# Kernel optimization log

Hardware: AMD Instinct MI355X
Metric: run time of the kernel (lower is better)

The kernel has to match this reference:

```python
import jax, jax.numpy as jnp
import numpy as np

B, T, C, H, N, FF = 2, 1024, 2048, 32, 64, 8192
DIV = 8.0  # head_size_divisor
LAYER_ID, N_LAYER = 1, 24
EPS = 1e-5


def _layer_norm(x, g, b):
    m = x.mean(-1, keepdims=True)
    v = x.var(-1, keepdims=True)
    return (x - m) / jnp.sqrt(v + EPS) * g + b


def _group_norm(x, g, b):
    # GroupNorm(H, C) applied per token: normalize each head's N channels
    xg = x.reshape(B, T, H, N)
    m = xg.mean(-1, keepdims=True)
    v = xg.var(-1, keepdims=True)
    xn = ((xg - m) / jnp.sqrt(v + EPS)).reshape(B, T, C)
    return xn * g + b


def _time_shift(x):
    # xx[t] = x[t-1], xx[0] = 0
    return jnp.pad(x, ((0, 0), (1, 0), (0, 0)))[:, :-1]


def _wkv5(r, k, v, w, u):
    # r,k,v: [B,T,H,N]; w,u: [H,N]. Linear recurrence with per-channel decay.
    decay = jnp.exp(-jnp.exp(w))            # [H,N]
    dec = decay[None, :, :, None]           # broadcast over B and v-dim
    uu = u[None, :, :, None]
    rs = jnp.moveaxis(r, 1, 0)              # [T,B,H,N]
    ks = jnp.moveaxis(k, 1, 0)
    vs = jnp.moveaxis(v, 1, 0)

    def step(state, inp):                   # state: [B,H,N,N] (k-dim i, v-dim j)
        rt, kt, vt = inp
        kv = kt[..., :, None] * vt[..., None, :]          # [B,H,N,N]
        y = jnp.einsum('bhi,bhij->bhj', rt, uu * kv + state)
        return dec * state + kv, y

    state0 = jnp.zeros((B, H, N, N), r.dtype)
    _, ys = jax.lax.scan(step, state0, (rs, ks, vs))
    return jnp.moveaxis(ys, 0, 1).reshape(B, T, C)


def _forward(x, ln1_g, ln1_b, ln2_g, ln2_b,
             tm_k, tm_v, tm_r, tm_g, time_decay, time_faaaa,
             Wr, Wk, Wv, Wg, Wo, lnx_g, lnx_b,
             fm_k, fm_r, Wkey, Wrec, Wval):
    # ---- TimeMix ----
    xl = _layer_norm(x, ln1_g, ln1_b)
    xx = _time_shift(xl)
    xk = xl * tm_k + xx * (1 - tm_k)
    xv = xl * tm_v + xx * (1 - tm_v)
    xr = xl * tm_r + xx * (1 - tm_r)
    xg = xl * tm_g + xx * (1 - tm_g)
    r = (xr @ Wr).reshape(B, T, H, N)
    k = (xk @ Wk).reshape(B, T, H, N)
    v = (xv @ Wv).reshape(B, T, H, N)
    g = jax.nn.silu(xg @ Wg)
    att = _wkv5(r, k, v, time_decay, time_faaaa)
    att = _group_norm(att / DIV, lnx_g, lnx_b)
    x = x + (att * g) @ Wo
    # ---- ChannelMix ----
    xl2 = _layer_norm(x, ln2_g, ln2_b)
    xx2 = _time_shift(xl2)
    ck = xl2 * fm_k + xx2 * (1 - fm_k)
    cr = xl2 * fm_r + xx2 * (1 - fm_r)
    kk = jnp.square(jax.nn.relu(ck @ Wkey))
    kv = kk @ Wval
    return x + jax.nn.sigmoid(cr @ Wrec) * kv


def setup_inputs() -> dict:
    key = jax.random.key(0)
    ks = jax.random.split(key, 9)
    r01 = LAYER_ID / (N_LAYER - 1)
    r1a0 = 1.0 - LAYER_ID / N_LAYER
    ddd = (np.arange(C, dtype=np.float64) / C)[None, None, :]
    dec = np.array([-6 + 5 * (n / (C - 1)) ** (0.7 + 1.3 * r01) for n in range(C)])
    faa = np.array([r01 * (1 - n / (C - 1)) + ((n + 1) % 3 - 1) * 0.1 for n in range(C)])
    f32 = lambda a: jnp.asarray(a, jnp.float32)
    w = lambda k_, i, o: jax.random.normal(k_, (i, o), jnp.float32) * (i ** -0.5)
    return {
        'x': jax.random.normal(ks[0], (B, T, C), jnp.float32),
        'ln1_g': jnp.ones((C,), jnp.float32), 'ln1_b': jnp.zeros((C,), jnp.float32),
        'ln2_g': jnp.ones((C,), jnp.float32), 'ln2_b': jnp.zeros((C,), jnp.float32),
        'tm_k': f32(ddd ** r1a0), 'tm_v': f32(ddd ** r1a0 + 0.3 * r01),
        'tm_r': f32(ddd ** (0.5 * r1a0)), 'tm_g': f32(ddd ** (0.5 * r1a0)),
        'time_decay': f32(dec.reshape(H, N)), 'time_faaaa': f32(faa.reshape(H, N)),
        'Wr': w(ks[1], C, C), 'Wk': w(ks[2], C, C), 'Wv': w(ks[3], C, C),
        'Wg': w(ks[4], C, C), 'Wo': w(ks[5], C, C),
        'lnx_g': jnp.ones((C,), jnp.float32), 'lnx_b': jnp.zeros((C,), jnp.float32),
        'fm_k': f32(ddd ** r1a0), 'fm_r': f32(ddd ** r1a0),
        'Wkey': w(ks[6], C, FF), 'Wrec': w(ks[7], C, C), 'Wval': w(ks[8], FF, C),
    }


def reference(x, ln1_g, ln1_b, ln2_g, ln2_b,
              tm_k, tm_v, tm_r, tm_g, time_decay, time_faaaa,
              Wr, Wk, Wv, Wg, Wo, lnx_g, lnx_b,
              fm_k, fm_r, Wkey, Wrec, Wval):
    return _forward(x, ln1_g, ln1_b, ln2_g, ln2_b,
                    tm_k, tm_v, tm_r, tm_g, time_decay, time_faaaa,
                    Wr, Wk, Wv, Wg, Wo, lnx_g, lnx_b,
                    fm_k, fm_r, Wkey, Wrec, Wval)
```

## Files before the change

### kernel.cpp

```cpp
#include <hip/hip_runtime.h>
#include <stdint.h>

#define BB 2
#define TT 1024
#define CC 2048
#define HH 32
#define NNH 64
#define FFD 8192
#define MTOT (BB*TT)
#define LNEPS 1e-5f
#define LOG2E 1.44269504088896340736f

typedef __attribute__((ext_vector_type(8))) __bf16 bf16x8;
typedef __attribute__((ext_vector_type(4))) float f32x4;

#define USE_GLL 1
typedef __attribute__((address_space(1))) void GAS;
typedef __attribute__((address_space(3))) void LAS;

__device__ inline void gload_lds16(const uint16_t* g, uint16_t* l) {
#if USE_GLL
  __builtin_amdgcn_global_load_lds((GAS*)g, (LAS*)l, 16, 0, 0);
#else
  *(uint4*)l = *(const uint4*)g;
#endif
}

__device__ inline float bf2f(uint32_t u) {
  union { uint32_t i; float f; } v; v.i = u << 16; return v.f;
}
__device__ inline uint16_t f2bf(float f) {
  union { float f; uint32_t i; } v; v.f = f;
  uint32_t r = v.i + 0x7FFFu + ((v.i >> 16) & 1u);
  return (uint16_t)(r >> 16);
}
__device__ inline void unpack8(uint4 d, float* v) {
  v[0] = bf2f(d.x & 0xffffu); v[1] = bf2f(d.x >> 16);
  v[2] = bf2f(d.y & 0xffffu); v[3] = bf2f(d.y >> 16);
  v[4] = bf2f(d.z & 0xffffu); v[5] = bf2f(d.z >> 16);
  v[6] = bf2f(d.w & 0xffffu); v[7] = bf2f(d.w >> 16);
}
__device__ inline uint4 pack8(const float* v) {
  uint4 d;
  d.x = (uint32_t)f2bf(v[0]) | ((uint32_t)f2bf(v[1]) << 16);
  d.y = (uint32_t)f2bf(v[2]) | ((uint32_t)f2bf(v[3]) << 16);
  d.z = (uint32_t)f2bf(v[4]) | ((uint32_t)f2bf(v[5]) << 16);
  d.w = (uint32_t)f2bf(v[6]) | ((uint32_t)f2bf(v[7]) << 16);
  return d;
}

__device__ inline void load8f(const void* p, size_t idx, int fl, float* v) {
  if (fl) {
    const float* q = (const float*)p + idx;
    float4 a = *(const float4*)q; float4 b = *(const float4*)(q + 4);
    v[0]=a.x; v[1]=a.y; v[2]=a.z; v[3]=a.w; v[4]=b.x; v[5]=b.y; v[6]=b.z; v[7]=b.w;
  } else {
    unpack8(*(const uint4*)((const uint16_t*)p + idx), v);
  }
}
__device__ inline float load1f(const void* p, size_t idx, int fl) {
  return fl ? ((const float*)p)[idx] : bf2f(((const uint16_t*)p)[idx]);
}

__global__ void probe_kernel(const uint16_t* __restrict__ x, int* __restrict__ flag) {
  int tid = threadIdx.x;
  float m = 0.f;
  for (int i = tid; i < 4096; i += 64) {
    float a = fabsf(bf2f(x[i]));
    if (a > m) m = a;
  }
  for (int o = 32; o; o >>= 1) { float t = __shfl_down(m, o); if (t > m) m = t; }
  if (tid == 0) *flag = (m > 1e6f) ? 1 : 0;
}

template<int INMODE>
__global__ __launch_bounds__(256) void ln_kernel(const void* __restrict__ x,
    const void* __restrict__ g, const void* __restrict__ b,
    uint16_t* __restrict__ out, const int* __restrict__ dflag)
{
  int fl = *dflag;
  int row = blockIdx.x;
  int tid = threadIdx.x;
  int lane = tid & 63, wave = tid >> 6;
  size_t base = (size_t)row * CC + (size_t)tid * 8;
  float v[8];
  if constexpr (INMODE == 1) {
    const float* q = (const float*)x + base;
    float4 a = *(const float4*)q; float4 c = *(const float4*)(q + 4);
    v[0]=a.x; v[1]=a.y; v[2]=a.z; v[3]=a.w; v[4]=c.x; v[5]=c.y; v[6]=c.z; v[7]=c.w;
  } else {
    load8f(x, base, fl, v);
  }
  float s = 0.f, s2 = 0.f;
  #pragma unroll
  for (int j = 0; j < 8; j++) { s += v[j]; s2 += v[j] * v[j]; }
  for (int o = 32; o; o >>= 1) { s += __shfl_down(s, o); s2 += __shfl_down(s2, o); }
  __shared__ float red[8];
  if (lane == 0) { red[wave] = s; red[wave + 4] = s2; }
  __syncthreads();
  s  = red[0] + red[1] + red[2] + red[3];
  s2 = red[4] + red[5] + red[6] + red[7];
  float mean = s * (1.0f / CC);
  float var  = s2 * (1.0f / CC) - mean * mean;
  float rstd = rsqrtf(fmaxf(var, 0.f) + LNEPS);
  float gj[8], bj[8];
  load8f(g, (size_t)tid * 8, fl, gj);
  load8f(b, (size_t)tid * 8, fl, bj);
  float o8[8];
  #pragma unroll
  for (int j = 0; j < 8; j++) o8[j] = (v[j] - mean) * rstd * gj[j] + bj[j];
  *(uint4*)(out + base) = pack8(o8);
}

__global__ __launch_bounds__(256) void mix4_kernel(const uint16_t* __restrict__ xl,
    const void* __restrict__ tmr, const void* __restrict__ tmk,
    const void* __restrict__ tmv, const void* __restrict__ tmg,
    uint16_t* __restrict__ out, const int* __restrict__ dflag)
{
  int fl = *dflag;
  uint32_t idx = ((uint32_t)blockIdx.x * 256u + threadIdx.x) * 8u;
  uint32_t c = idx & (CC - 1);
  uint32_t row = idx >> 11;
  uint32_t t = row & (TT - 1);
  float xv[8], pv[8];
  unpack8(*(const uint4*)(xl + idx), xv);
  if (t) { unpack8(*(const uint4*)(xl + idx - CC), pv); }
  else   { for (int j = 0; j < 8; j++) pv[j] = 0.f; }
  const void* tms[4] = { tmr, tmk, tmv, tmg };
  const size_t SL = (size_t)MTOT * CC;
  #pragma unroll
  for (int a = 0; a < 4; a++) {
    float tm[8], o[8];
    load8f(tms[a], c, fl, tm);
    #pragma unroll
    for (int j = 0; j < 8; j++) o[j] = xv[j] * tm[j] + pv[j] * (1.f - tm[j]);
    *(uint4*)(out + a * SL + idx) = pack8(o);
  }
}

__global__ __launch_bounds__(256) void mix2_kernel(const uint16_t* __restrict__ xl,
    const void* __restrict__ tk, const void* __restrict__ tr,
    uint16_t* __restrict__ ok, uint16_t* __restrict__ orr,
    const int* __restrict__ dflag)
{
  int fl = *dflag;
  uint32_t idx = ((uint32_t)blockIdx.x * 256u + threadIdx.x) * 8u;
  uint32_t c = idx & (CC - 1);
  uint32_t row = idx >> 11;
  uint32_t t = row & (TT - 1);
  float xv[8], pv[8], tm[8], o[8];
  unpack8(*(const uint4*)(xl + idx), xv);
  if (t) { unpack8(*(const uint4*)(xl + idx - CC), pv); }
  else   { for (int j = 0; j < 8; j++) pv[j] = 0.f; }
  load8f(tk, c, fl, tm);
  #pragma unroll
  for (int j = 0; j < 8; j++) o[j] = xv[j] * tm[j] + pv[j] * (1.f - tm[j]);
  *(uint4*)(ok + idx) = pack8(o);
  load8f(tr, c, fl, tm);
  #pragma unroll
  for (int j = 0; j < 8; j++) o[j] = xv[j] * tm[j] + pv[j] * (1.f - tm[j]);
  *(uint4*)(orr + idx) = pack8(o);
}

__device__ inline void transpose_tile(const void* W, uint16_t* WT, int Kd, int Nd,
                                      int n0, int k0, int fl, int tid)
{
  __shared__ __align__(16) uint16_t tile[64][66];
  int r = tid >> 3, s = tid & 7;
  #pragma unroll
  for (int p = 0; p < 2; p++) {
    int row = p * 32 + r;
    float tv[8];
    load8f(W, (size_t)(k0 + row) * Nd + n0 + s * 8, fl, tv);
    uint16_t* t = &tile[row][s * 8];
    #pragma unroll
    for (int e = 0; e < 8; e++) t[e] = f2bf(tv[e]);
  }
  __syncthreads();
  #pragma unroll
  for (int p = 0; p < 2; p++) {
    int row = p * 32 + r;
    uint16_t tmp[8];
    #pragma unroll
    for (int e = 0; e < 8; e++) tmp[e] = tile[s * 8 + e][row];
    uint4 o;
    o.x = (uint32_t)tmp[0] | ((uint32_t)tmp[1] << 16);
    o.y = (uint32_t)tmp[2] | ((uint32_t)tmp[3] << 16);
    o.z = (uint32_t)tmp[4] | ((uint32_t)tmp[5] << 16);
    o.w = (uint32_t)tmp[6] | ((uint32_t)tmp[7] << 16);
    *(uint4*)(WT + (size_t)(n0 + row) * Kd + k0 + s * 8) = o;
  }
}

__global__ __launch_bounds__(256) void transpose_kernel(const void* __restrict__ W,
    uint16_t* __restrict__ WT, int Kd, int Nd, const int* __restrict__ dflag)
{
  transpose_tile(W, WT, Kd, Nd, blockIdx.x * 64, blockIdx.y * 64, *dflag, threadIdx.x);
}

__global__ __launch_bounds__(256) void transpose4_kernel(
    const void* __restrict__ W0, const void* __restrict__ W1,
    const void* __restrict__ W2, const void* __restrict__ W3,
    uint16_t* __restrict__ WT, const int* __restrict__ dflag)
{
  const void* Ws[4] = { W0, W1, W2, W3 };
  int z = blockIdx.z;
  transpose_tile(Ws[z], WT + (size_t)z * CC * CC, CC, CC,
                 blockIdx.x * 64, blockIdx.y * 64, *dflag, threadIdx.x);
}

enum { EPI_RESID = 2, EPI_RKVG = 6, EPI_FF2 = 7, EPI_PART = 8 };

template<int EPI>
__global__ __launch_bounds__(256, 2) void gemm_kernel(
    const uint16_t* __restrict__ Ain, const uint16_t* __restrict__ BTin,
    void* __restrict__ Cout, int N, int Kstride, int Kloop,
    const void* __restrict__ auxA, const float* __restrict__ auxf,
    const uint16_t* __restrict__ A2in, const uint16_t* __restrict__ BT2in,
    void* __restrict__ C2out, const int* __restrict__ dflag)
{
  const uint16_t* A  = Ain;
  const uint16_t* BT = BTin;
  uint16_t* co16 = (uint16_t*)Cout;
  float*    co32 = (float*)Cout;
  int fl = 0;
  if constexpr (EPI == EPI_RESID) fl = *dflag;
  bool silu = false, sigm = false;
  int bx = blockIdx.x;
  int N_ = N;
  int n0 = bx * 128;
  if constexpr (EPI == EPI_RKVG) {
    int z = blockIdx.z;
    A    += (size_t)z * MTOT * CC;
    BT   += (size_t)z * CC * CC;
    co16 += (size_t)z * MTOT * CC;
    silu = (z == 3);
  }
  if constexpr (EPI == EPI_PART) {
    int z = blockIdx.z;
    A    += (size_t)z * Kloop;
    BT   += (size_t)z * Kloop;
    co32 += (size_t)z * MTOT * 2048;
  }
  if constexpr (EPI == EPI_FF2) {
    if (bx >= 64) {
      n0 = (bx - 64) * 128;
      A = A2in; BT = BT2in; co16 = (uint16_t*)C2out; N_ = 2048; sigm = true;
    }
  }
  int m0 = blockIdx.y * 128;
  __shared__ __align__(16) uint16_t As[128 * 64];
  __shared__ __align__(16) uint16_t Bs[128 * 64];
  int tid = threadIdx.x;
  int lane = tid & 63, wave = tid >> 6;
  int wm = (wave >> 1) * 64, wn = (wave & 1) * 64;
  int l15 = lane & 15, lq = lane >> 4;
  int sw = l15 & 7;
  f32x4 acc[4][4];
  #pragma unroll
  for (int i = 0; i < 4; i++)
    #pragma unroll
    for (int j = 0; j < 4; j++) acc[i][j] = 0.f;
  const int rr = tid >> 3, seg = tid & 7;
  const int sseg = (seg ^ (rr & 7)) * 8;
  const uint16_t* Ag = A + (size_t)(m0 + rr) * Kstride + sseg;
  const uint16_t* Bg = BT + (size_t)(n0 + rr) * Kstride + sseg;
  uint16_t* Asw = As + tid * 8;
  uint16_t* Bsw = Bs + tid * 8;
  for (int k0 = 0; k0 < Kloop; k0 += 64) {
    __syncthreads();
    #pragma unroll
    for (int p = 0; p < 4; p++) {
      gload_lds16(Ag + (size_t)p * 32 * Kstride + k0, Asw + p * 2048);
      gload_lds16(Bg + (size_t)p * 32 * Kstride + k0, Bsw + p * 2048);
    }
    __syncthreads();
    #pragma unroll
    for (int kk = 0; kk < 2; kk++) {
      int cidx = ((kk * 4 + lq) ^ sw) * 8;
      bf16x8 af[4], bv[4];
      #pragma unroll
      for (int f = 0; f < 4; f++) af[f] = *(const bf16x8*)&As[(wm + f * 16 + l15) * 64 + cidx];
      #pragma unroll
      for (int f = 0; f < 4; f++) bv[f] = *(const bf16x8*)&Bs[(wn + f * 16 + l15) * 64 + cidx];
      #pragma unroll
      for (int fm = 0; fm < 4; fm++)
        #pragma unroll
        for (int fn = 0; fn < 4; fn++)
          acc[fm][fn] = __builtin_amdgcn_mfma_f32_16x16x32_bf16(af[fm], bv[fn], acc[fm][fn], 0, 0, 0);
    }
  }
  #pragma unroll
  for (int fm = 0; fm < 4; fm++) {
    #pragma unroll
    for (int q = 0; q < 4; q++) {
      int gr = m0 + wm + fm * 16 + lq * 4 + q;
      size_t rowb = (size_t)gr * N_;
      #pragma unroll
      for (int fn = 0; fn < 4; fn++) {
        int gc = n0 + wn + fn * 16 + l15;
        size_t idx = rowb + gc;
        float val = acc[fm][fn][q];
        if constexpr (EPI == EPI_RKVG) {
          if (silu) val = val / (1.f + __expf(-fmaxf(val, -80.f)));
          co16[idx] = f2bf(val);
        } else if constexpr (EPI == EPI_RESID) {
          co32[idx] = val + load1f(auxA, idx, fl);
        } else if constexpr (EPI == EPI_FF2) {
          if (sigm) {
            co16[idx] = f2bf(1.f / (1.f + __expf(-val)));
          } else {
            float t = fmaxf(val, 0.f);
            co16[idx] = f2bf(t * t);
          }
        } else if constexpr (EPI == EPI_PART) {
          co32[idx] = val;
        }
      }
    }
  }
}

__global__ __launch_bounds__(256) void final_reduce_kernel(
    const float* __restrict__ P, const float* __restrict__ x1,
    const uint16_t* __restrict__ sr, void* __restrict__ out,
    const int* __restrict__ dflag)
{
  int fl = *dflag;
  size_t idx = ((size_t)blockIdx.x * 256 + threadIdx.x) * 8;
  const float* P1 = P + (size_t)MTOT * 2048;
  float a[8], b[8], xv[8], s8[8], o[8];
  { float4 t0 = *(const float4*)(P + idx);  float4 t1 = *(const float4*)(P + idx + 4);
    a[0]=t0.x;a[1]=t0.y;a[2]=t0.z;a[3]=t0.w;a[4]=t1.x;a[5]=t1.y;a[6]=t1.z;a[7]=t1.w; }
  { float4 t0 = *(const float4*)(P1 + idx); float4 t1 = *(const float4*)(P1 + idx + 4);
    b[0]=t0.x;b[1]=t0.y;b[2]=t0.z;b[3]=t0.w;b[4]=t1.x;b[5]=t1.y;b[6]=t1.z;b[7]=t1.w; }
  { float4 t0 = *(const float4*)(x1 + idx); float4 t1 = *(const float4*)(x1 + idx + 4);
    xv[0]=t0.x;xv[1]=t0.y;xv[2]=t0.z;xv[3]=t0.w;xv[4]=t1.x;xv[5]=t1.y;xv[6]=t1.z;xv[7]=t1.w; }
  unpack8(*(const uint4*)(sr + idx), s8);
  #pragma unroll
  for (int j = 0; j < 8; j++) o[j] = xv[j] + s8[j] * (a[j] + b[j]);
  if (fl) {
    float* q = (float*)out + idx;
    *(float4*)q = make_float4(o[0], o[1], o[2], o[3]);
    *(float4*)(q + 4) = make_float4(o[4], o[5], o[6], o[7]);
  } else {
    *(uint4*)((uint16_t*)out + idx) = pack8(o);
  }
}

__global__ __launch_bounds__(256) void wkv_p_kernel(
    const uint16_t* __restrict__ kq, const uint16_t* __restrict__ vq,
    const void* __restrict__ wq, float* __restrict__ P,
    const int* __restrict__ dflag)
{
  int fl = *dflag;
  int blk = blockIdx.x;
  int c = blk & 15, h = (blk >> 4) & 31, b = blk >> 9;
  __shared__ __align__(16) float Kt[64][64];
  __shared__ __align__(16) uint16_t Vb[64][64];
  __shared__ __align__(16) float e_s[64];
  int tid = threadIdx.x;
  if (tid < 64) e_s[tid] = fminf(__expf(load1f(wq, h * 64 + tid, fl)), 100.f);
  __syncthreads();
  int rr = tid >> 3, cs = (tid & 7) * 8;
  #pragma unroll
  for (int p = 0; p < 2; p++) {
    int s = p * 32 + rr;
    size_t gbase = ((size_t)(b * TT + c * 64 + s)) * CC + h * 64 + cs;
    float k8[8];
    unpack8(*(const uint4*)(kq + gbase), k8);
    float sp = (float)(s + 1) * LOG2E;
    #pragma unroll
    for (int j = 0; j < 8; j++) Kt[s][cs + j] = k8[j] * exp2f(fminf(sp * e_s[cs + j], 80.f));
    *(uint4*)&Vb[s][cs] = *(const uint4*)(vq + gbase);
  }
  __syncthreads();
  int tx = tid & 15, ty = tid >> 4;
  int i0 = ty * 4, j0 = tx * 4;
  float acc[4][4] = {};
  for (int s = 0; s < 64; s++) {
    float4 a = *(const float4*)&Kt[s][i0];
    ushort4 vv = *(const ushort4*)&Vb[s][j0];
    float b0 = bf2f(vv.x), b1 = bf2f(vv.y), b2 = bf2f(vv.z), b3 = bf2f(vv.w);
    float am[4] = { a.x, a.y, a.z, a.w };
    #pragma unroll
    for (int m = 0; m < 4; m++) {
      acc[m][0] += am[m] * b0; acc[m][1] += am[m] * b1;
      acc[m][2] += am[m] * b2; acc[m][3] += am[m] * b3;
    }
  }
  float* Pb = P + (size_t)blk * 4096;
  #pragma unroll
  for (int m = 0; m < 4; m++) {
    float dl = exp2f(-64.0f * LOG2E * e_s[i0 + m]);
    float4 o = { acc[m][0] * dl, acc[m][1] * dl, acc[m][2] * dl, acc[m][3] * dl };
    *(float4*)&Pb[(i0 + m) * 64 + j0] = o;
  }
}

__global__ __launch_bounds__(256) void wkv_s_kernel(const float* __restrict__ P,
    const void* __restrict__ wq, float* __restrict__ S,
    const int* __restrict__ dflag)
{
  int fl = *dflag;
  int bh = blockIdx.x;
  int h = bh & 31;
  int tid = threadIdx.x;
  int i = tid >> 2, q = tid & 3;
  float e = fminf(__expf(load1f(wq, h * 64 + i, fl)), 100.f);
  float dl = exp2f(-64.0f * LOG2E * e);
  float4 s0 = {0,0,0,0}, s1 = {0,0,0,0}, s2 = {0,0,0,0}, s3 = {0,0,0,0};
  for (int c = 0; c < 16; c++) {
    size_t base = ((size_t)bh * 16 + c) * 4096 + (size_t)i * 64 + q * 16;
    *(float4*)&S[base + 0]  = s0;
    *(float4*)&S[base + 4]  = s1;
    *(float4*)&S[base + 8]  = s2;
    *(float4*)&S[base + 12] = s3;
    float4 p0 = *(const float4*)&P[base + 0];
    float4 p1 = *(const float4*)&P[base + 4];
    float4 p2 = *(const float4*)&P[base + 8];
    float4 p3 = *(const float4*)&P[base + 12];
    s0 = make_float4(dl * s0.x + p0.x, dl * s0.y + p0.y, dl * s0.z + p0.z, dl * s0.w + p0.w);
    s1 = make_float4(dl * s1.x + p1.x, dl * s1.y + p1.y, dl * s1.z + p1.z, dl * s1.w + p1.w);
    s2 = make_float4(dl * s2.x + p2.x, dl * s2.y + p2.y, dl * s2.z + p2.z, dl * s2.w + p2.w);
    s3 = make_float4(dl * s3.x + p3.x, dl * s3.y + p3.y, dl * s3.z + p3.z, dl * s3.w + p3.w);
  }
}

__global__ __launch_bounds__(256, 2) void wkv_y_kernel(
    const uint16_t* __restrict__ rq, const uint16_t* __restrict__ kq,
    const uint16_t* __restrict__ vq, const void* __restrict__ wq,
    const void* __restrict__ uq, const float* __restrict__ S,
    float* __restrict__ att, const int* __restrict__ dflag)
{
  int fl = *dflag;
  int blk = blockIdx.x;
  int c = blk & 15, h = (blk >> 4) & 31, b = blk >> 9;
  __shared__ __align__(16) float Rt[64][64];
  __shared__ __align__(16) float Kt[64][64];
  __shared__ __align__(16) uint16_t Vb[64][64];
  __shared__ __align__(16) float Ss[64][64];
  __shared__ __align__(16) float e_s[64];
  __shared__ __align__(16) float ud_s[64];
  int tid = threadIdx.x;
  if (tid < 64) {
    float e = fminf(__expf(load1f(wq, h * 64 + tid, fl)), 100.f);
    e_s[tid] = e;
    ud_s[tid] = load1f(uq, h * 64 + tid, fl) * __expf(-e);
  }
  __syncthreads();
  int rr = tid >> 3, cs = (tid & 7) * 8;
  #pragma unroll
  for (int p = 0; p < 2; p++) {
    int s = p * 32 + rr;
    size_t gbase = ((size_t)(b * TT + c * 64 + s)) * CC + h * 64 + cs;
    float r8[8], k8[8];
    unpack8(*(const uint4*)(rq + gbase), r8);
    unpack8(*(const uint4*)(kq + gbase), k8);
    float tneg = -(float)s * LOG2E;
    float spos = (float)(s + 1) * LOG2E;
    #pragma unroll
    for (int j = 0; j < 8; j++) {
      float e = e_s[cs + j];
      Rt[s][cs + j] = r8[j] * exp2f(tneg * e);
      Kt[s][cs + j] = k8[j] * exp2f(fminf(spos * e, 80.f));
    }
    *(uint4*)&Vb[s][cs] = *(const uint4*)(vq + gbase);
  }
  {
    int r2 = tid >> 2, q = tid & 3;
    const float* Sbp = S + (size_t)blk * 4096 + (size_t)r2 * 64 + q * 16;
    *(float4*)&Ss[r2][q * 16 + 0]  = *(const float4*)&Sbp[0];
    *(float4*)&Ss[r2][q * 16 + 4]  = *(const float4*)&Sbp[4];
    *(float4*)&Ss[r2][q * 16 + 8]  = *(const float4*)&Sbp[8];
    *(float4*)&Ss[r2][q * 16 + 12] = *(const float4*)&Sbp[12];
  }
  __syncthreads();
  int tx = tid & 15, ty = tid >> 4;
  int t0 = ty * 4, s0 = tx * 4;
  float acc[4][4] = {};
  for (int iq = 0; iq < 16; iq++) {
    int i = iq * 4;
    float4 ra[4], kb[4];
    #pragma unroll
    for (int m = 0; m < 4; m++) ra[m] = *(const float4*)&Rt[t0 + m][i];
    #pragma unroll
    for (int n = 0; n < 4; n++) kb[n] = *(const float4*)&Kt[s0 + n][i];
    #pragma unroll
    for (int m = 0; m < 4; m++)
      #pragma unroll
      for (int n = 0; n < 4; n++)
        acc[m][n] += ra[m].x * kb[n].x + ra[m].y * kb[n].y + ra[m].z * kb[n].z + ra[m].w * kb[n].w;
  }
  float dg = 0.f;
  if (tid < 64) {
    for (int iq = 0; iq < 16; iq++) {
      int i = iq * 4;
      float4 a = *(const float4*)&Rt[tid][i];
      float4 kk = *(const float4*)&Kt[tid][i];
      float4 u4 = *(const float4*)&ud_s[i];
      dg += a.x * kk.x * u4.x + a.y * kk.y * u4.y + a.z * kk.z * u4.z + a.w * kk.w * u4.w;
    }
  }
  __syncthreads();
  #pragma unroll
  for (int m = 0; m < 4; m++)
    #pragma unroll
    for (int n = 0; n < 4; n++) {
      int t = t0 + m, s = s0 + n;
      Kt[t][s] = (s < t) ? acc[m][n] : 0.0f;
    }
  __syncthreads();
  if (tid < 64) Kt[tid][tid] = dg;
  __syncthreads();
  int j0 = tx * 4;
  float y[4][4] = {};
  for (int sq = 0; sq < 16; sq++) {
    int s = sq * 4;
    float4 a4[4];
    #pragma unroll
    for (int m = 0; m < 4; m++) a4[m] = *(const float4*)&Kt[t0 + m][s];
    float vb[4][4];
    #pragma unroll
    for (int qq = 0; qq < 4; qq++) {
      ushort4 vv = *(const ushort4*)&Vb[s + qq][j0];
      vb[qq][0] = bf2f(vv.x); vb[qq][1] = bf2f(vv.y); vb[qq][2] = bf2f(vv.z); vb[qq][3] = bf2f(vv.w);
    }
    #pragma unroll
    for (int m = 0; m < 4; m++)
      #pragma unroll
      for (int n = 0; n < 4; n++)
        y[m][n] += a4[m].x * vb[0][n] + a4[m].y * vb[1][n] + a4[m].z * vb[2][n] + a4[m].w * vb[3][n];
  }
  for (int iq = 0; iq < 16; iq++) {
    int i = iq * 4;
    float4 r4[4], s4[4];
    #pragma unroll
    for (int m = 0; m < 4; m++) r4[m] = *(const float4*)&Rt[t0 + m][i];
    #pragma unroll
    for (int qq = 0; qq < 4; qq++) s4[qq] = *(const float4*)&Ss[i + qq][j0];
    #pragma unroll
    for (int m = 0; m < 4; m++)
      #pragma unroll
      for (int n = 0; n < 4; n++)
        y[m][n] += r4[m].x * s4[0][n] + r4[m].y * s4[1][n] + r4[m].z * s4[2][n] + r4[m].w * s4[3][n];
  }
  #pragma unroll
  for (int m = 0; m < 4; m++) {
    size_t ob = ((size_t)(b * TT + c * 64 + t0 + m)) * CC + h * 64 + j0;
    *(float4*)&att[ob] = make_float4(y[m][0], y[m][1], y[m][2], y[m][3]);
  }
}

__global__ __launch_bounds__(256) void gn_mul_kernel(const float* __restrict__ att,
    const void* __restrict__ gg, const void* __restrict__ bb,
    const uint16_t* __restrict__ gate, uint16_t* __restrict__ out,
    const int* __restrict__ dflag)
{
  int fl = *dflag;
  int row = blockIdx.x;
  int tid = threadIdx.x;
  size_t base = (size_t)row * CC + (size_t)tid * 8;
  float4 a0 = *(const float4*)(att + base);
  float4 a1 = *(const float4*)(att + base + 4);
  float v[8] = { a0.x, a0.y, a0.z, a0.w, a1.x, a1.y, a1.z, a1.w };
  #pragma unroll
  for (int j = 0; j < 8; j++) v[j] *= 0.125f;
  float s = 0.f, s2 = 0.f;
  #pragma unroll
  for (int j = 0; j < 8; j++) { s += v[j]; s2 += v[j] * v[j]; }
  s += __shfl_xor(s, 1); s += __shfl_xor(s, 2); s += __shfl_xor(s, 4);
  s2 += __shfl_xor(s2, 1); s2 += __shfl_xor(s2, 2); s2 += __shfl_xor(s2, 4);
  float m = s * (1.f / 64.f);
  float var = s2 * (1.f / 64.f) - m * m;
  float rstd = rsqrtf(fmaxf(var, 0.f) + LNEPS);
  int c = tid * 8;
  float g8[8], b8[8], gt8[8], o[8];
  load8f(gg, c, fl, g8);
  load8f(bb, c, fl, b8);
  unpack8(*(const uint4*)(gate + base), gt8);
  #pragma unroll
  for (int j = 0; j < 8; j++) o[j] = ((v[j] - m) * rstd * g8[j] + b8[j]) * gt8[j];
  *(uint4*)(out + base) = pack8(o);
}

extern "C" void kernel_launch(void* const* d_in, const int* in_sizes, int n_in,
                              void* d_out, int out_size, void* d_ws, size_t ws_size,
                              hipStream_t stream)
{
  const void* x    = d_in[0];
  const void* ln1g = d_in[1];
  const void* ln1b = d_in[2];
  const void* ln2g = d_in[3];
  const void* ln2b = d_in[4];
  const void* tmk  = d_in[5];
  const void* tmv  = d_in[6];
  const void* tmr  = d_in[7];
  const void* tmg  = d_in[8];
  const void* tdec = d_in[9];
  const void* tfaa = d_in[10];
  const void* Wr   = d_in[11];
  const void* Wk   = d_in[12];
  const void* Wv   = d_in[13];
  const void* Wg   = d_in[14];
  const void* Wo   = d_in[15];
  const void* lnxg = d_in[16];
  const void* lnxb = d_in[17];
  const void* fmk  = d_in[18];
  const void* fmr  = d_in[19];
  const void* Wkey = d_in[20];
  const void* Wrec = d_in[21];
  const void* Wval = d_in[22];

  char* ws = (char*)d_ws;
  const size_t SL  = (size_t)MTOT * CC;
  const size_t SLW = (size_t)CC * CC;
  uint16_t* XL    = (uint16_t*)(ws + 0);
  uint16_t* WRECT = XL;
  uint16_t* MIX4  = (uint16_t*)(ws + 8388608);
  float*    PART  = (float*)   (ws + 8388608);
  uint16_t* RKVG  = (uint16_t*)(ws + 41943040);
  float*    ATT   = (float*)   (ws + 75497472);
  float*    X1    = ATT;
  float*    Pb    = (float*)   (ws + 92274688);
  float*    Sb    = (float*)   (ws + 109051904);
  uint16_t* KK    = (uint16_t*)(ws + 92274688);
  uint16_t* WT    = (uint16_t*)(ws + 125829120);
  int*      FLAG  = (int*)     (ws + 159383552);
  (void)in_sizes; (void)n_in; (void)out_size; (void)ws_size;

  probe_kernel<<<dim3(1), 64, 0, stream>>>((const uint16_t*)x, FLAG);
  ln_kernel<0><<<dim3(MTOT), 256, 0, stream>>>(x, ln1g, ln1b, XL, FLAG);
  transpose4_kernel<<<dim3(32, 32, 4), 256, 0, stream>>>(Wr, Wk, Wv, Wg, WT, FLAG);
  mix4_kernel<<<dim3(2048), 256, 0, stream>>>(XL, tmr, tmk, tmv, tmg, MIX4, FLAG);
  gemm_kernel<EPI_RKVG><<<dim3(16, 16, 4), 256, 0, stream>>>(MIX4, WT, (void*)RKVG, CC, CC, CC,
      nullptr, nullptr, nullptr, nullptr, nullptr, FLAG);
  wkv_p_kernel<<<dim3(1024), 256, 0, stream>>>(RKVG + 1 * SL, RKVG + 2 * SL, tdec, Pb, FLAG);
  wkv_s_kernel<<<dim3(64), 256, 0, stream>>>(Pb, tdec, Sb, FLAG);
  wkv_y_kernel<<<dim3(1024), 256, 0, stream>>>(RKVG + 0 * SL, RKVG + 1 * SL, RKVG + 2 * SL, tdec, tfaa, Sb, ATT, FLAG);
  gn_mul_kernel<<<dim3(MTOT), 256, 0, stream>>>(ATT, lnxg, lnxb, RKVG + 3 * SL, MIX4, FLAG);
  transpose_kernel<<<dim3(32, 32), 256, 0, stream>>>(Wo, WT, CC, CC, FLAG);
  gemm_kernel<EPI_RESID><<<dim3(16, 16), 256, 0, stream>>>(MIX4, WT, (void*)X1, CC, CC, CC,
      x, nullptr, nullptr, nullptr, nullptr, FLAG);
  ln_kernel<1><<<dim3(MTOT), 256, 0, stream>>>(X1, ln2g, ln2b, XL, FLAG);
  mix2_kernel<<<dim3(2048), 256, 0, stream>>>(XL, fmk, fmr, MIX4, RKVG, FLAG);
  transpose_kernel<<<dim3(FFD / 64, CC / 64), 256, 0, stream>>>(Wkey, WT, CC, FFD, FLAG);
  transpose_kernel<<<dim3(32, 32), 256, 0, stream>>>(Wrec, WRECT, CC, CC, FLAG);
  gemm_kernel<EPI_FF2><<<dim3(80, 16), 256, 0, stream>>>(MIX4, WT, (void*)KK, FFD, CC, CC,
      nullptr, nullptr, RKVG, WRECT, (void*)(RKVG + 2 * SL), FLAG);
  transpose_kernel<<<dim3(CC / 64, FFD / 64), 256, 0, stream>>>(Wval, WT, FFD, CC, FLAG);
  gemm_kernel<EPI_PART><<<dim3(16, 16, 2), 256, 0, stream>>>(KK, WT, (void*)PART, CC, FFD, FFD / 2,
      nullptr, nullptr, nullptr, nullptr, nullptr, FLAG);
  final_reduce_kernel<<<dim3(2048), 256, 0, stream>>>(PART, X1, RKVG + 2 * SL, d_out, FLAG);
}
```

Baseline: 740.3 us.

## Add 256x256 tiled 512-thread GEMM with pipelined LDS staging for large matmuls

Introduces a new 512-thread GEMM kernel with 256x256 output tiles, double-buffered direct global-to-LDS loads interleaved with MFMA quadrants and priority hints, and uses it for the RKVG projections, the FFN key GEMM, and the FFN value GEMM. The value GEMM's split-K goes from 2 to 4 partitions, with extra partial buffers placed in reused workspace regions, and the final reduce sums four partials. The receptance GEMM is split out from the fused FF2 launch into its own sigmoid-epilogue launch. The goal is higher arithmetic intensity and less LDS/global traffic per FLOP, at the cost of more LDS use, lower occupancy, fewer blocks per GEMM, and an extra launch.

```diff
diff --git a/kernel.cpp b/kernel.cpp
--- a/kernel.cpp
+++ b/kernel.cpp
@@ -209,15 +209,13 @@
                  blockIdx.x * 64, blockIdx.y * 64, *dflag, threadIdx.x);
 }
 
-enum { EPI_RESID = 2, EPI_RKVG = 6, EPI_FF2 = 7, EPI_PART = 8 };
+enum { EPI_RESID = 2, EPI_SIGM = 9 };
 
 template<int EPI>
 __global__ __launch_bounds__(256, 2) void gemm_kernel(
     const uint16_t* __restrict__ Ain, const uint16_t* __restrict__ BTin,
     void* __restrict__ Cout, int N, int Kstride, int Kloop,
-    const void* __restrict__ auxA, const float* __restrict__ auxf,
-    const uint16_t* __restrict__ A2in, const uint16_t* __restrict__ BT2in,
-    void* __restrict__ C2out, const int* __restrict__ dflag)
+    const void* __restrict__ auxA, const int* __restrict__ dflag)
 {
   const uint16_t* A  = Ain;
   const uint16_t* BT = BTin;
@@ -225,29 +223,9 @@
   float*    co32 = (float*)Cout;
   int fl = 0;
   if constexpr (EPI == EPI_RESID) fl = *dflag;
-  bool silu = false, sigm = false;
   int bx = blockIdx.x;
   int N_ = N;
   int n0 = bx * 128;
-  if constexpr (EPI == EPI_RKVG) {
-    int z = blockIdx.z;
-    A    += (size_t)z * MTOT * CC;
-    BT   += (size_t)z * CC * CC;
-    co16 += (size_t)z * MTOT * CC;
-    silu = (z == 3);
-  }
-  if constexpr (EPI == EPI_PART) {
-    int z = blockIdx.z;
-    A    += (size_t)z * Kloop;
-    BT   += (size_t)z * Kloop;
-    co32 += (size_t)z * MTOT * 2048;
-  }
-  if constexpr (EPI == EPI_FF2) {
-    if (bx >= 64) {
-      n0 = (bx - 64) * 128;
-      A = A2in; BT = BT2in; co16 = (uint16_t*)C2out; N_ = 2048; sigm = true;
-    }
-  }
   int m0 = blockIdx.y * 128;
   __shared__ __align__(16) uint16_t As[128 * 64];
   __shared__ __align__(16) uint16_t Bs[128 * 64];
@@ -301,44 +279,223 @@
         int gc = n0 + wn + fn * 16 + l15;
         size_t idx = rowb + gc;
         float val = acc[fm][fn][q];
-        if constexpr (EPI == EPI_RKVG) {
-          if (silu) val = val / (1.f + __expf(-fmaxf(val, -80.f)));
-          co16[idx] = f2bf(val);
-        } else if constexpr (EPI == EPI_RESID) {
+        if constexpr (EPI == EPI_RESID) {
           co32[idx] = val + load1f(auxA, idx, fl);
-        } else if constexpr (EPI == EPI_FF2) {
-          if (sigm) {
-            co16[idx] = f2bf(1.f / (1.f + __expf(-val)));
-          } else {
-            float t = fmaxf(val, 0.f);
-            co16[idx] = f2bf(t * t);
-          }
-        } else if constexpr (EPI == EPI_PART) {
-          co32[idx] = val;
+        } else if constexpr (EPI == EPI_SIGM) {
+          co16[idx] = f2bf(1.f / (1.f + __expf(-val)));
         }
       }
     }
   }
 }
 
+enum { G_RKVG = 0, G_KK = 1, G_PART = 2 };
+
+template<int EPI>
+__global__ __launch_bounds__(512, 2) void gemm256_kernel(
+    const uint16_t* __restrict__ Ain, const uint16_t* __restrict__ BTin,
+    void* __restrict__ Cout, int N, int Kstride, int Kloop,
+    float* __restrict__ p2, float* __restrict__ p3a, float* __restrict__ p3b)
+{
+  __shared__ __align__(16) uint16_t smem[65536];
+  const uint16_t* A  = Ain;
+  const uint16_t* BT = BTin;
+  uint16_t* co16 = (uint16_t*)Cout;
+  float*    co32 = (float*)Cout;
+  int n0 = blockIdx.x * 256;
+  int m0 = blockIdx.y * 256;
+  bool silu = false;
+  if constexpr (EPI == G_RKVG) {
+    int z = blockIdx.z;
+    A    += (size_t)z * MTOT * CC;
+    BT   += (size_t)z * CC * CC;
+    co16 += (size_t)z * MTOT * CC;
+    silu = (z == 3);
+  }
+  if constexpr (EPI == G_PART) {
+    int z = blockIdx.z;
+    A  += (size_t)z * Kloop;
+    BT += (size_t)z * Kloop;
+    if (z < 2)      co32 += (size_t)z * MTOT * 2048;
+    else if (z == 2) co32 = p2;
+    else            co32 = (m0 < 1024) ? p3a : (p3b - (size_t)1024 * 2048);
+  }
+  const int tid  = threadIdx.x;
+  const int lane = tid & 63, wave = tid >> 6;
+  const int wm = wave >> 2;
+  const int wn = wave & 3;
+  const int l15 = lane & 15, lq = lane >> 4;
+  const int sw = l15 & 7;
+  const int c0 = ((0 * 4 + lq) ^ sw) * 8;
+  const int c1 = ((1 * 4 + lq) ^ sw) * 8;
+
+  const int trow = tid >> 3;
+  const int tswz = ((tid & 7) ^ (trow & 7)) * 8;
+  const uint16_t* Ag = A  + ((size_t)m0 + trow) * Kstride + tswz;
+  const uint16_t* Bg = BT + ((size_t)n0 + trow) * Kstride + tswz;
+  uint16_t* ldsT = smem + tid * 8;
+  const size_t r64K = (size_t)64 * Kstride;
+
+  const uint16_t* aRd = smem + (wm * 64 + l15) * 64;
+  const uint16_t* bRd = smem + 32768 + (wn * 32 + l15) * 64;
+
+  bf16x8 a[4][2];
+  bf16x8 bb[2][2][2];
+  f32x4  acc[2][4][2][2];
+  #pragma unroll
+  for (int mh = 0; mh < 2; mh++)
+    #pragma unroll
+    for (int f = 0; f < 4; f++)
+      #pragma unroll
+      for (int nh = 0; nh < 2; nh++)
+        #pragma unroll
+        for (int g = 0; g < 2; g++) acc[mh][f][nh][g] = 0.f;
+
+#define STG(Mg, matOff, d, h, kt) do { \
+    const uint16_t* s_ = (Mg) + (size_t)((h) * 128) * Kstride + (size_t)(kt) * 64; \
+    uint16_t* l_ = ldsT + (matOff) + (d) * 16384 + (h) * 8192; \
+    gload_lds16(s_, l_); \
+    gload_lds16(s_ + r64K, l_ + 4096); \
+  } while (0)
+
+#define RD_A(mh, d) do { \
+    const uint16_t* p_ = aRd + (d) * 16384 + (mh) * 8192; \
+    _Pragma("unroll") \
+    for (int f = 0; f < 4; f++) { \
+      a[f][0] = *(const bf16x8*)(p_ + f * 1024 + c0); \
+      a[f][1] = *(const bf16x8*)(p_ + f * 1024 + c1); \
+    } \
+  } while (0)
+
+#define RD_B(nh, d) do { \
+    const uint16_t* p_ = bRd + (d) * 16384 + (nh) * 8192; \
+    _Pragma("unroll") \
+    for (int g = 0; g < 2; g++) { \
+      bb[nh][g][0] = *(const bf16x8*)(p_ + g * 1024 + c0); \
+      bb[nh][g][1] = *(const bf16x8*)(p_ + g * 1024 + c1); \
+    } \
+  } while (0)
+
+#define QUAD(mh, nh) do { \
+    __builtin_amdgcn_s_setprio(1); \
+    _Pragma("unroll") \
+    for (int f = 0; f < 4; f++) \
+      _Pragma("unroll") \
+      for (int g = 0; g < 2; g++) { \
+        acc[mh][f][nh][g] = __builtin_amdgcn_mfma_f32_16x16x32_bf16(a[f][0], bb[nh][g][0], acc[mh][f][nh][g], 0, 0, 0); \
+        acc[mh][f][nh][g] = __builtin_amdgcn_mfma_f32_16x16x32_bf16(a[f][1], bb[nh][g][1], acc[mh][f][nh][g], 0, 0, 0); \
+      } \
+    __builtin_amdgcn_s_setprio(0); \
+  } while (0)
+
+#define TILE(t, d) do { \
+     \
+    RD_A(0, d); RD_B(0, d); \
+    if ((t) + 1 < NT) STG(Ag, 0, (d) ^ 1, 1, (t) + 1); \
+    __builtin_amdgcn_s_barrier(); \
+    asm volatile("s_waitcnt lgkmcnt(0)" ::: "memory"); \
+    QUAD(0, 0); \
+    __builtin_amdgcn_s_barrier(); \
+     \
+    RD_B(1, d); \
+    if ((t) + 2 < NT) STG(Ag, 0, d, 0, (t) + 2); \
+    __builtin_amdgcn_s_barrier(); \
+    asm volatile("s_waitcnt lgkmcnt(0)" ::: "memory"); \
+    QUAD(0, 1); \
+    __builtin_amdgcn_s_barrier(); \
+     \
+    RD_A(1, d); \
+    if ((t) + 2 < NT) STG(Bg, 32768, d, 0, (t) + 2); \
+    __builtin_amdgcn_s_barrier(); \
+    asm volatile("s_waitcnt lgkmcnt(0)" ::: "memory"); \
+    QUAD(1, 1); \
+    __builtin_amdgcn_s_barrier(); \
+     \
+    if ((t) + 2 < NT) STG(Bg, 32768, d, 1, (t) + 2); \
+    __builtin_amdgcn_s_barrier(); \
+    QUAD(1, 0); \
+    if ((t) + 2 < NT)      { asm volatile("s_waitcnt vmcnt(6)" ::: "memory"); } \
+    else if ((t) + 1 < NT) { asm volatile("s_waitcnt vmcnt(0)" ::: "memory"); } \
+    __builtin_amdgcn_s_barrier(); \
+  } while (0)
+
+  const int NT = Kloop >> 6;
+  STG(Ag, 0, 0, 0, 0); STG(Ag, 0, 0, 1, 0);
+  STG(Bg, 32768, 0, 0, 0); STG(Bg, 32768, 0, 1, 0);
+  if (NT > 1) {
+    STG(Ag, 0, 1, 0, 1); STG(Bg, 32768, 1, 0, 1); STG(Bg, 32768, 1, 1, 1);
+    asm volatile("s_waitcnt vmcnt(6)" ::: "memory");
+  } else {
+    asm volatile("s_waitcnt vmcnt(0)" ::: "memory");
+  }
+  __builtin_amdgcn_s_barrier();
+
+  for (int t = 0; t < NT; t += 2) {
+    TILE(t, 0);
+    TILE(t + 1, 1);
+  }
+
+#undef TILE
+#undef QUAD
+#undef RD_B
+#undef RD_A
+#undef STG
+
+  #pragma unroll
+  for (int mh = 0; mh < 2; mh++) {
+    #pragma unroll
+    for (int f = 0; f < 4; f++) {
+      #pragma unroll
+      for (int q = 0; q < 4; q++) {
+        int gr = m0 + mh * 128 + wm * 64 + f * 16 + lq * 4 + q;
+        size_t rowb = (size_t)gr * N;
+        #pragma unroll
+        for (int nh = 0; nh < 2; nh++) {
+          #pragma unroll
+          for (int g = 0; g < 2; g++) {
+            int gc = n0 + nh * 128 + wn * 32 + g * 16 + l15;
+            size_t idx = rowb + gc;
+            float val = acc[mh][f][nh][g][q];
+            if constexpr (EPI == G_RKVG) {
+              if (silu) val = val / (1.f + __expf(-fmaxf(val, -80.f)));
+              co16[idx] = f2bf(val);
+            } else if constexpr (EPI == G_KK) {
+              float tv = fmaxf(val, 0.f);
+              co16[idx] = f2bf(tv * tv);
+            } else if constexpr (EPI == G_PART) {
+              co32[idx] = val;
+            }
+          }
+        }
+      }
+    }
+  }
+}
+
 __global__ __launch_bounds__(256) void final_reduce_kernel(
     const float* __restrict__ P, const float* __restrict__ x1,
     const uint16_t* __restrict__ sr, void* __restrict__ out,
-    const int* __restrict__ dflag)
+    const float* __restrict__ P2, const float* __restrict__ P3a,
+    const float* __restrict__ P3b, const int* __restrict__ dflag)
 {
   int fl = *dflag;
   size_t idx = ((size_t)blockIdx.x * 256 + threadIdx.x) * 8;
   const float* P1 = P + (size_t)MTOT * 2048;
-  float a[8], b[8], xv[8], s8[8], o[8];
+  const float* P3 = (idx < (size_t)1024 * 2048) ? (P3a + idx) : (P3b + idx - (size_t)1024 * 2048);
+  float a[8], b[8], c2[8], d3[8], xv[8], s8[8], o[8];
   { float4 t0 = *(const float4*)(P + idx);  float4 t1 = *(const float4*)(P + idx + 4);
     a[0]=t0.x;a[1]=t0.y;a[2]=t0.z;a[3]=t0.w;a[4]=t1.x;a[5]=t1.y;a[6]=t1.z;a[7]=t1.w; }
   { float4 t0 = *(const float4*)(P1 + idx); float4 t1 = *(const float4*)(P1 + idx + 4);
     b[0]=t0.x;b[1]=t0.y;b[2]=t0.z;b[3]=t0.w;b[4]=t1.x;b[5]=t1.y;b[6]=t1.z;b[7]=t1.w; }
+  { float4 t0 = *(const float4*)(P2 + idx); float4 t1 = *(const float4*)(P2 + idx + 4);
+    c2[0]=t0.x;c2[1]=t0.y;c2[2]=t0.z;c2[3]=t0.w;c2[4]=t1.x;c2[5]=t1.y;c2[6]=t1.z;c2[7]=t1.w; }
+  { float4 t0 = *(const float4*)(P3);       float4 t1 = *(const float4*)(P3 + 4);
+    d3[0]=t0.x;d3[1]=t0.y;d3[2]=t0.z;d3[3]=t0.w;d3[4]=t1.x;d3[5]=t1.y;d3[6]=t1.z;d3[7]=t1.w; }
   { float4 t0 = *(const float4*)(x1 + idx); float4 t1 = *(const float4*)(x1 + idx + 4);
     xv[0]=t0.x;xv[1]=t0.y;xv[2]=t0.z;xv[3]=t0.w;xv[4]=t1.x;xv[5]=t1.y;xv[6]=t1.z;xv[7]=t1.w; }
   unpack8(*(const uint4*)(sr + idx), s8);
   #pragma unroll
-  for (int j = 0; j < 8; j++) o[j] = xv[j] + s8[j] * (a[j] + b[j]);
+  for (int j = 0; j < 8; j++) o[j] = xv[j] + s8[j] * (a[j] + b[j] + c2[j] + d3[j]);
   if (fl) {
     float* q = (float*)out + idx;
     *(float4*)q = make_float4(o[0], o[1], o[2], o[3]);
@@ -614,7 +771,6 @@
 
   char* ws = (char*)d_ws;
   const size_t SL  = (size_t)MTOT * CC;
-  const size_t SLW = (size_t)CC * CC;
   uint16_t* XL    = (uint16_t*)(ws + 0);
   uint16_t* WRECT = XL;
   uint16_t* MIX4  = (uint16_t*)(ws + 8388608);
@@ -633,23 +789,26 @@
   ln_kernel<0><<<dim3(MTOT), 256, 0, stream>>>(x, ln1g, ln1b, XL, FLAG);
   transpose4_kernel<<<dim3(32, 32, 4), 256, 0, stream>>>(Wr, Wk, Wv, Wg, WT, FLAG);
   mix4_kernel<<<dim3(2048), 256, 0, stream>>>(XL, tmr, tmk, tmv, tmg, MIX4, FLAG);
-  gemm_kernel<EPI_RKVG><<<dim3(16, 16, 4), 256, 0, stream>>>(MIX4, WT, (void*)RKVG, CC, CC, CC,
-      nullptr, nullptr, nullptr, nullptr, nullptr, FLAG);
+  gemm256_kernel<G_RKVG><<<dim3(8, 8, 4), 512, 0, stream>>>(MIX4, WT, (void*)RKVG, CC, CC, CC,
+      nullptr, nullptr, nullptr);
   wkv_p_kernel<<<dim3(1024), 256, 0, stream>>>(RKVG + 1 * SL, RKVG + 2 * SL, tdec, Pb, FLAG);
   wkv_s_kernel<<<dim3(64), 256, 0, stream>>>(Pb, tdec, Sb, FLAG);
   wkv_y_kernel<<<dim3(1024), 256, 0, stream>>>(RKVG + 0 * SL, RKVG + 1 * SL, RKVG + 2 * SL, tdec, tfaa, Sb, ATT, FLAG);
   gn_mul_kernel<<<dim3(MTOT), 256, 0, stream>>>(ATT, lnxg, lnxb, RKVG + 3 * SL, MIX4, FLAG);
   transpose_kernel<<<dim3(32, 32), 256, 0, stream>>>(Wo, WT, CC, CC, FLAG);
   gemm_kernel<EPI_RESID><<<dim3(16, 16), 256, 0, stream>>>(MIX4, WT, (void*)X1, CC, CC, CC,
-      x, nullptr, nullptr, nullptr, nullptr, FLAG);
+      x, FLAG);
   ln_kernel<1><<<dim3(MTOT), 256, 0, stream>>>(X1, ln2g, ln2b, XL, FLAG);
   mix2_kernel<<<dim3(2048), 256, 0, stream>>>(XL, fmk, fmr, MIX4, RKVG, FLAG);
   transpose_kernel<<<dim3(FFD / 64, CC / 64), 256, 0, stream>>>(Wkey, WT, CC, FFD, FLAG);
   transpose_kernel<<<dim3(32, 32), 256, 0, stream>>>(Wrec, WRECT, CC, CC, FLAG);
-  gemm_kernel<EPI_FF2><<<dim3(80, 16), 256, 0, stream>>>(MIX4, WT, (void*)KK, FFD, CC, CC,
-      nullptr, nullptr, RKVG, WRECT, (void*)(RKVG + 2 * SL), FLAG);
+  gemm256_kernel<G_KK><<<dim3(32, 8), 512, 0, stream>>>(MIX4, WT, (void*)KK, FFD, CC, CC,
+      nullptr, nullptr, nullptr);
+  gemm_kernel<EPI_SIGM><<<dim3(16, 16), 256, 0, stream>>>(RKVG, WRECT, (void*)(RKVG + 2 * SL), CC, CC, CC,
+      nullptr, FLAG);
   transpose_kernel<<<dim3(CC / 64, FFD / 64), 256, 0, stream>>>(Wval, WT, FFD, CC, FLAG);
-  gemm_kernel<EPI_PART><<<dim3(16, 16, 2), 256, 0, stream>>>(KK, WT, (void*)PART, CC, FFD, FFD / 2,
-      nullptr, nullptr, nullptr, nullptr, nullptr, FLAG);
-  final_reduce_kernel<<<dim3(2048), 256, 0, stream>>>(PART, X1, RKVG + 2 * SL, d_out, FLAG);
-}
+  gemm256_kernel<G_PART><<<dim3(8, 8, 4), 512, 0, stream>>>(KK, WT, (void*)PART, CC, FFD, FFD / 4,
+      (float*)RKVG, (float*)XL, (float*)(RKVG + 3 * SL));
+  final_reduce_kernel<<<dim3(2048), 256, 0, stream>>>(PART, X1, RKVG + 2 * SL, d_out,
+      (float*)RKVG, (float*)XL, (float*)(RKVG + 3 * SL), FLAG);
+}
```

Measured after the change: 726.6 us. No clear change (-1.8%).
